# Kernel tuning notes

Hardware: AMD Instinct MI355X
Metric: run time of the kernel (lower is better)

## Reference

```python
import jax, jax.numpy as jnp
import numpy as np

DIV_EPS = 1e-7   # epsilon in dense_div denominator (as in source)
POW_EPS = 1e-7   # clamp for pow base to avoid nan (0^negative); see notes
N_OPS = 7        # [zero, one(bug:also zero), add, minus, mul, div, pow]


def setup_inputs() -> dict:
    B, S = 4096, 256
    key = jax.random.key(0)
    k1, k2, k3 = jax.random.split(key, 3)
    trans_valid = (jax.random.uniform(k1, (B, S)) < 0.7).astype(jnp.float32)
    # positive dense values so pow(h1, h0) stays real
    trans_dense = jax.random.uniform(k2, (B, S), dtype=jnp.float32)
    trans_op = jax.random.normal(k3, (B, S, N_OPS), dtype=jnp.float32)
    if_finished = jnp.zeros((B,), jnp.float32)
    if_valid = jnp.ones((B,), jnp.float32)
    return {
        "trans_valid": trans_valid,
        "trans_dense": trans_dense,
        "trans_op": trans_op,
        "if_finished": if_finished,
        "if_valid": if_valid,
        "start_pos": 0,
    }


def _shift(h):
    # matmul with next_mask ([[0,1],[0,0]]): [h0, h1] -> [0, h0]
    return jnp.stack([jnp.zeros_like(h[:, 0]), h[:, 0]], axis=-1)


def _forward(trans_valid, trans_dense, trans_op, if_finished, if_valid, start_pos):
    B, S = trans_valid.shape
    dt = trans_valid.dtype
    hold_numbers = jnp.zeros((B, 2), dt)
    hold_status = jnp.zeros((B, 2), dt)
    hold_index = jnp.zeros((B, 2), jnp.int32)
    meet_op = jnp.zeros((B,), dt)

    def step(carry, xs):
        hn, hs, hi, meet, iv, tv, td = carry
        i, op_i = xs  # i scalar, op_i [B, N_OPS]
        active = (i >= start_pos).astype(dt)  # steps before start_pos are no-ops
        tv_i = jnp.take(tv, i, axis=1)  # trans_valid[:, i]
        td_i = jnp.take(td, i, axis=1)  # trans_dense[:, i]
        itv = tv_i * (1 - meet) * (1 - if_finished) * active
        oh = jax.nn.one_hot(jnp.argmax(op_i, axis=-1), N_OPS, dtype=dt)  # [B,7]
        not_op_gate = oh[:, 0]
        dag = iv * not_op_gate * itv  # dense_applied_gate [B]
        d = dag[:, None]
        hn = d * _shift(hn) + (1 - d) * hn
        hs = d * _shift(hs) + (1 - d) * hs
        gi = dag.astype(jnp.int32)  # truncation, matches .long()
        gic = gi[:, None]
        hi = gic * jnp.stack([jnp.zeros_like(hi[:, 0]), hi[:, 0]], -1) + (1 - gic) * hi
        hi = hi.at[:, 0].set(hi[:, 0] * (1 - gi) + gi * i)
        hs = hs.at[:, 0].set(hs[:, 0] * (1 - dag) + dag)
        hn = hn.at[:, 0].set(hn[:, 0] * (1 - dag) + dag * td_i)
        op_gate = (1 - not_op_gate) * itv * iv
        meet = op_gate * (1 - meet) + meet
        iv = op_gate * hs[:, 0] * hs[:, 1] + (1 - op_gate) * iv
        h0, h1 = hn[:, 0], hn[:, 1]
        zero = jnp.zeros_like(h0)
        dense_ops = jnp.stack(
            [zero, zero,  # dense_zero, dense_one (source bug: one == zero)
             h1 + h0, h1 - h0, h1 * h0,
             h1 / (h0 + DIV_EPS),
             jnp.power(jnp.maximum(h1, POW_EPS), h0)], axis=-1)  # [B,7]
        dense_calc = jnp.sum(dense_ops * oh, axis=-1)
        fg = (1 - not_op_gate) * itv * iv  # final_op_gate (uses updated iv)
        oh2 = jax.nn.one_hot(hi[:, 0], S, dtype=dt)  # number2 position
        oh1 = jax.nn.one_hot(hi[:, 1], S, dtype=dt)  # number1 position
        fgc = fg[:, None]
        tv = tv * (1 - fgc) + tv * fgc * (1 - oh1)
        td = td * (1 - fgc) + td * fgc * (1 - oh2) + dense_calc[:, None] * fgc * oh2
        tv = tv.at[:, i].multiply(1 - fg)
        hs = hs.at[:, 0].multiply(1 - fg)
        return (hn, hs, hi, meet, iv, tv, td), None

    xs = (jnp.arange(S), jnp.moveaxis(trans_op, 1, 0))  # ([S], [S,B,7])
    carry = (hold_numbers, hold_status, hold_index, meet_op, if_valid, trans_valid, trans_dense)
    (hn, hs, hi, meet, iv, tv, td), _ = jax.lax.scan(step, carry, xs)
    ifu = iv * (1 - meet) * hs[:, 0] * (1 - hs[:, 1])
    iff = (1 - if_finished) * ifu + if_finished
    return tv, td, trans_op, iff, iv


def reference(trans_valid, trans_dense, trans_op, if_finished, if_valid, start_pos):
    return _forward(trans_valid, trans_dense, trans_op, if_finished, if_valid, start_pos)
```

## Files before the change

kernel.cpp:

```cpp
#include <hip/hip_runtime.h>

#define BB 4096
#define SS 256
#define NOPS 7

typedef float f32x4 __attribute__((ext_vector_type(4)));

__global__ __launch_bounds__(256) void arth_kernel(
    const float* __restrict__ tv_in,
    const float* __restrict__ td_in,
    const float* __restrict__ op_in,
    const float* __restrict__ if_fin,
    const float* __restrict__ if_val,
    const int* __restrict__ start_pos_p,
    float* __restrict__ out_tv,
    float* __restrict__ out_td,
    float* __restrict__ out_op,
    float* __restrict__ out_iff,
    float* __restrict__ out_iv)
{
    __shared__ float s_op[SS * NOPS];
    __shared__ float s_td[SS];
    __shared__ unsigned char s_amax[SS];
    __shared__ unsigned long long sm_op[4];
    __shared__ unsigned long long sm_num[4];

    const int b = blockIdx.x;
    const int t = threadIdx.x;
    const size_t rbase = (size_t)b * SS;
    const size_t obase = (size_t)b * (SS * NOPS);

    const int start_pos = *start_pos_p;
    const float fin_f = if_fin[b];
    const float iv0 = if_val[b];

    const f32x4* in4 = (const f32x4*)(op_in + obase);
    f32x4* o4 = (f32x4*)(out_op + obase);
    f32x4* s4 = (f32x4*)s_op;

    f32x4 v0 = in4[t];
    f32x4 v1;
    if (t < 192) v1 = in4[256 + t];
    const float tvv = tv_in[rbase + t];
    const float tdv = td_in[rbase + t];

    o4[t] = v0;
    s4[t] = v0;
    if (t < 192) {
        o4[256 + t] = v1;
        s4[256 + t] = v1;
    }
    s_td[t] = tdv;
    __syncthreads();

    int am = 0;
    float best = s_op[t * NOPS];
    #pragma unroll
    for (int k = 1; k < NOPS; ++k) {
        float v = s_op[t * NOPS + k];
        if (v > best) { best = v; am = k; }
    }
    s_amax[t] = (unsigned char)am;

    const bool validtok = (t >= start_pos) && (tvv > 0.5f);
    const bool is_num = validtok && (am == 0);
    const bool is_op = validtok && (am != 0);

    unsigned long long mo = __ballot(is_op);
    unsigned long long mn = __ballot(is_num);
    if ((t & 63) == 0) {
        sm_op[t >> 6] = mo;
        sm_num[t >> 6] = mn;
    }
    __syncthreads();

    unsigned long long w_op0 = sm_op[0], w_op1 = sm_op[1], w_op2 = sm_op[2], w_op3 = sm_op[3];
    unsigned long long w_nm[4] = { sm_num[0], sm_num[1], sm_num[2], sm_num[3] };

    int j = -1;
    if (w_op0)      j = __builtin_ctzll(w_op0);
    else if (w_op1) j = 64 + __builtin_ctzll(w_op1);
    else if (w_op2) j = 128 + __builtin_ctzll(w_op2);
    else if (w_op3) j = 192 + __builtin_ctzll(w_op3);

    int i0 = -1, i1 = -1;
    #pragma unroll
    for (int ww = 3; ww >= 0; --ww) {
        if (i1 >= 0) continue;
        unsigned long long m = w_nm[ww];
        if (j >= 0) {
            int jw = j - ww * 64;
            if (jw <= 0) m = 0ull;
            else if (jw < 64) m &= ((1ull << jw) - 1ull);
        }
        while (m && i1 < 0) {
            int bit = 63 - __builtin_clzll(m);
            if (i0 < 0) i0 = ww * 64 + bit;
            else        i1 = ww * 64 + bit;
            m &= ~(1ull << bit);
        }
    }

    const bool finished = fin_f > 0.5f;
    const bool valid0 = iv0 > 0.5f;

    float otv = tvv, otd = tdv;
    float iff, ivout;
    if (finished) {
        iff = 1.0f;
        ivout = iv0;
    } else if (!valid0) {
        iff = 0.0f;
        ivout = 0.0f;
    } else if (j < 0) {
        ivout = 1.0f;
        iff = (i0 >= 0 && i1 < 0) ? 1.0f : 0.0f;
    } else if (i1 >= 0) {
        float h0 = s_td[i0];
        float h1 = s_td[i1];
        int op = s_amax[j];
        float res;
        switch (op) {
            case 2: res = h1 + h0; break;
            case 3: res = h1 - h0; break;
            case 4: res = h1 * h0; break;
            case 5: res = h1 / (h0 + 1e-7f); break;
            case 6: res = powf(fmaxf(h1, 1e-7f), h0); break;
            default: res = 0.0f; break;
        }
        if (t == i0) otd = res;
        if (t == i1 || t == j) otv = 0.0f;
        ivout = 1.0f;
        iff = 0.0f;
    } else {
        ivout = 0.0f;
        iff = 0.0f;
    }

    out_tv[rbase + t] = otv;
    out_td[rbase + t] = otd;
    if (t == 0) {
        out_iff[b] = iff;
        out_iv[b] = ivout;
    }
}

extern "C" void kernel_launch(void* const* d_in, const int* in_sizes, int n_in,
                              void* d_out, int out_size, void* d_ws, size_t ws_size,
                              hipStream_t stream) {
    const float* tv_in = (const float*)d_in[0];
    const float* td_in = (const float*)d_in[1];
    const float* op_in = (const float*)d_in[2];
    const float* if_fin = (const float*)d_in[3];
    const float* if_val = (const float*)d_in[4];
    const int* start_pos = (const int*)d_in[5];

    float* out = (float*)d_out;
    float* out_tv = out;
    float* out_td = out + (size_t)BB * SS;
    float* out_op = out + (size_t)2 * BB * SS;
    float* out_iff = out + (size_t)9 * BB * SS;
    float* out_iv = out + (size_t)9 * BB * SS + BB;

    arth_kernel<<<BB, SS, 0, stream>>>(tv_in, td_in, op_in, if_fin, if_val,
                                       start_pos, out_tv, out_td, out_op,
                                       out_iff, out_iv);
}
```

Before: 17.46 us.

## Process one row per wavefront with register-only ballots and shuffles

```diff
diff --git a/kernel.cpp b/kernel.cpp
--- a/kernel.cpp
+++ b/kernel.cpp
@@ -6,7 +6,15 @@
 
 typedef float f32x4 __attribute__((ext_vector_type(4)));
 
-__global__ __launch_bounds__(256) void arth_kernel(
+__device__ __forceinline__ float sel4(f32x4 v, int idx) {
+    float r = v.x;
+    r = (idx == 1) ? v.y : r;
+    r = (idx == 2) ? v.z : r;
+    r = (idx == 3) ? v.w : r;
+    return r;
+}
+
+__global__ __launch_bounds__(256, 4) void arth_kernel(
     const float* __restrict__ tv_in,
     const float* __restrict__ td_in,
     const float* __restrict__ op_in,
@@ -19,108 +27,131 @@
     float* __restrict__ out_iff,
     float* __restrict__ out_iv)
 {
-    __shared__ float s_op[SS * NOPS];
-    __shared__ float s_td[SS];
-    __shared__ unsigned char s_amax[SS];
-    __shared__ unsigned long long sm_op[4];
-    __shared__ unsigned long long sm_num[4];
-
-    const int b = blockIdx.x;
     const int t = threadIdx.x;
-    const size_t rbase = (size_t)b * SS;
-    const size_t obase = (size_t)b * (SS * NOPS);
+    const int wv = t >> 6;
+    const int l  = t & 63;
+    const int r  = (blockIdx.x << 2) + wv;
+    const size_t rbase = (size_t)r * SS;
+    const size_t obase = (size_t)r * (SS * NOPS);
 
     const int start_pos = *start_pos_p;
-    const float fin_f = if_fin[b];
-    const float iv0 = if_val[b];
+    const float fin_f = if_fin[r];
+    const float iv0   = if_val[r];
 
     const f32x4* in4 = (const f32x4*)(op_in + obase);
     f32x4* o4 = (f32x4*)(out_op + obase);
-    f32x4* s4 = (f32x4*)s_op;
-
-    f32x4 v0 = in4[t];
-    f32x4 v1;
-    if (t < 192) v1 = in4[256 + t];
-    const float tvv = tv_in[rbase + t];
-    const float tdv = td_in[rbase + t];
-
-    o4[t] = v0;
-    s4[t] = v0;
-    if (t < 192) {
-        o4[256 + t] = v1;
-        s4[256 + t] = v1;
-    }
-    s_td[t] = tdv;
-    __syncthreads();
-
-    int am = 0;
-    float best = s_op[t * NOPS];
-    #pragma unroll
-    for (int k = 1; k < NOPS; ++k) {
-        float v = s_op[t * NOPS + k];
-        if (v > best) { best = v; am = k; }
-    }
-    s_amax[t] = (unsigned char)am;
-
-    const bool validtok = (t >= start_pos) && (tvv > 0.5f);
-    const bool is_num = validtok && (am == 0);
-    const bool is_op = validtok && (am != 0);
-
-    unsigned long long mo = __ballot(is_op);
-    unsigned long long mn = __ballot(is_num);
-    if ((t & 63) == 0) {
-        sm_op[t >> 6] = mo;
-        sm_num[t >> 6] = mn;
-    }
-    __syncthreads();
-
-    unsigned long long w_op0 = sm_op[0], w_op1 = sm_op[1], w_op2 = sm_op[2], w_op3 = sm_op[3];
-    unsigned long long w_nm[4] = { sm_num[0], sm_num[1], sm_num[2], sm_num[3] };
-
-    int j = -1;
-    if (w_op0)      j = __builtin_ctzll(w_op0);
-    else if (w_op1) j = 64 + __builtin_ctzll(w_op1);
-    else if (w_op2) j = 128 + __builtin_ctzll(w_op2);
-    else if (w_op3) j = 192 + __builtin_ctzll(w_op3);
-
-    int i0 = -1, i1 = -1;
-    #pragma unroll
-    for (int ww = 3; ww >= 0; --ww) {
-        if (i1 >= 0) continue;
-        unsigned long long m = w_nm[ww];
-        if (j >= 0) {
-            int jw = j - ww * 64;
-            if (jw <= 0) m = 0ull;
-            else if (jw < 64) m &= ((1ull << jw) - 1ull);
-        }
-        while (m && i1 < 0) {
-            int bit = 63 - __builtin_clzll(m);
-            if (i0 < 0) i0 = ww * 64 + bit;
-            else        i1 = ww * 64 + bit;
-            m &= ~(1ull << bit);
+
+    f32x4 c0 = in4[l];
+    f32x4 c1 = in4[l + 64];
+    f32x4 c2 = in4[l + 128];
+    f32x4 c3 = in4[l + 192];
+    f32x4 c4 = in4[l + 256];
+    f32x4 c5 = in4[l + 320];
+    f32x4 c6 = in4[l + 384];
+    const f32x4* a4 = (const f32x4*)(op_in + obase + (size_t)l * 28);
+    f32x4 u0 = a4[0], u1 = a4[1], u2 = a4[2], u3 = a4[3];
+    f32x4 u4 = a4[4], u5 = a4[5], u6 = a4[6];
+    f32x4 tv4 = *(const f32x4*)(tv_in + rbase + (l << 2));
+    f32x4 td4 = *(const f32x4*)(td_in + rbase + (l << 2));
+
+    __builtin_nontemporal_store(c0, &o4[l]);
+    __builtin_nontemporal_store(c1, &o4[l + 64]);
+    __builtin_nontemporal_store(c2, &o4[l + 128]);
+    __builtin_nontemporal_store(c3, &o4[l + 192]);
+    __builtin_nontemporal_store(c4, &o4[l + 256]);
+    __builtin_nontemporal_store(c5, &o4[l + 320]);
+    __builtin_nontemporal_store(c6, &o4[l + 384]);
+
+    float af[28];
+    *(f32x4*)(af +  0) = u0; *(f32x4*)(af +  4) = u1;
+    *(f32x4*)(af +  8) = u2; *(f32x4*)(af + 12) = u3;
+    *(f32x4*)(af + 16) = u4; *(f32x4*)(af + 20) = u5;
+    *(f32x4*)(af + 24) = u6;
+
+    int am[4];
+    #pragma unroll
+    for (int k = 0; k < 4; ++k) {
+        const int base = k * NOPS;
+        int a = 0; float best = af[base];
+        #pragma unroll
+        for (int q = 1; q < NOPS; ++q) {
+            float v = af[base + q];
+            if (v > best) { best = v; a = q; }
+        }
+        am[k] = a;
+    }
+
+    unsigned long long bop[4], bnm[4];
+    #pragma unroll
+    for (int k = 0; k < 4; ++k) {
+        const int p = (l << 2) + k;
+        const bool vt = (p >= start_pos) && (sel4(tv4, k) > 0.5f);
+        bop[k] = __ballot(vt && (am[k] != 0));
+        bnm[k] = __ballot(vt && (am[k] == 0));
+    }
+
+    int j = 1 << 30;
+    #pragma unroll
+    for (int k = 0; k < 4; ++k)
+        if (bop[k]) { int c = (__builtin_ctzll(bop[k]) << 2) + k; j = (c < j) ? c : j; }
+    const bool hasop = (j < (1 << 30));
+
+    unsigned long long msk[4];
+    #pragma unroll
+    for (int k = 0; k < 4; ++k) {
+        unsigned long long mm = bnm[k];
+        if (hasop) {
+            int lim = j - 1 - k;
+            if (lim < 0) mm = 0ull;
+            else {
+                int lmax = lim >> 2;
+                mm &= (lmax >= 63) ? ~0ull : ((2ull << lmax) - 1ull);
+            }
+        }
+        msk[k] = mm;
+    }
+
+    int i0 = -1, k0 = -1;
+    #pragma unroll
+    for (int k = 0; k < 4; ++k)
+        if (msk[k]) {
+            int c = ((63 - __builtin_clzll(msk[k])) << 2) + k;
+            if (c > i0) { i0 = c; k0 = k; }
+        }
+    int i1 = -1;
+    if (i0 >= 0) {
+        #pragma unroll
+        for (int k = 0; k < 4; ++k) {
+            unsigned long long mm = msk[k];
+            if (k == k0) mm &= ~(1ull << (i0 >> 2));
+            if (mm) {
+                int c = ((63 - __builtin_clzll(mm)) << 2) + k;
+                if (c > i1) i1 = c;
+            }
         }
     }
 
     const bool finished = fin_f > 0.5f;
     const bool valid0 = iv0 > 0.5f;
 
-    float otv = tvv, otd = tdv;
     float iff, ivout;
     if (finished) {
-        iff = 1.0f;
-        ivout = iv0;
+        iff = 1.0f; ivout = iv0;
     } else if (!valid0) {
-        iff = 0.0f;
-        ivout = 0.0f;
-    } else if (j < 0) {
-        ivout = 1.0f;
-        iff = (i0 >= 0 && i1 < 0) ? 1.0f : 0.0f;
+        iff = 0.0f; ivout = 0.0f;
+    } else if (!hasop) {
+        ivout = 1.0f; iff = (i0 >= 0 && i1 < 0) ? 1.0f : 0.0f;
     } else if (i1 >= 0) {
-        float h0 = s_td[i0];
-        float h1 = s_td[i1];
-        int op = s_amax[j];
+        float h0 = __shfl(sel4(td4, i0 & 3), i0 >> 2, 64);
+        float h1 = __shfl(sel4(td4, i1 & 3), i1 >> 2, 64);
+        int av = am[0];
+        { int ks = j & 3;
+          av = (ks == 1) ? am[1] : av;
+          av = (ks == 2) ? am[2] : av;
+          av = (ks == 3) ? am[3] : av; }
+        int opj = __shfl(av, j >> 2, 64);
         float res;
-        switch (op) {
+        switch (opj) {
             case 2: res = h1 + h0; break;
             case 3: res = h1 - h0; break;
             case 4: res = h1 * h0; break;
@@ -128,20 +159,31 @@
             case 6: res = powf(fmaxf(h1, 1e-7f), h0); break;
             default: res = 0.0f; break;
         }
-        if (t == i0) otd = res;
-        if (t == i1 || t == j) otv = 0.0f;
-        ivout = 1.0f;
-        iff = 0.0f;
+        {
+            const bool me = (l == (i0 >> 2)); const int ci = i0 & 3;
+            td4.x = (me && ci == 0) ? res : td4.x;
+            td4.y = (me && ci == 1) ? res : td4.y;
+            td4.z = (me && ci == 2) ? res : td4.z;
+            td4.w = (me && ci == 3) ? res : td4.w;
+        }
+        {
+            const bool m1 = (l == (i1 >> 2)); const int c1 = i1 & 3;
+            const bool mj = (l == (j >> 2));  const int cj = j & 3;
+            tv4.x = ((m1 && c1 == 0) || (mj && cj == 0)) ? 0.0f : tv4.x;
+            tv4.y = ((m1 && c1 == 1) || (mj && cj == 1)) ? 0.0f : tv4.y;
+            tv4.z = ((m1 && c1 == 2) || (mj && cj == 2)) ? 0.0f : tv4.z;
+            tv4.w = ((m1 && c1 == 3) || (mj && cj == 3)) ? 0.0f : tv4.w;
+        }
+        ivout = 1.0f; iff = 0.0f;
     } else {
-        ivout = 0.0f;
-        iff = 0.0f;
-    }
-
-    out_tv[rbase + t] = otv;
-    out_td[rbase + t] = otd;
-    if (t == 0) {
-        out_iff[b] = iff;
-        out_iv[b] = ivout;
+        ivout = 0.0f; iff = 0.0f;
+    }
+
+    __builtin_nontemporal_store(tv4, (f32x4*)(out_tv + rbase + (l << 2)));
+    __builtin_nontemporal_store(td4, (f32x4*)(out_td + rbase + (l << 2)));
+    if (l == 0) {
+        out_iff[r] = iff;
+        out_iv[r] = ivout;
     }
 }
 
@@ -162,7 +204,7 @@
     float* out_iff = out + (size_t)9 * BB * SS;
     float* out_iv = out + (size_t)9 * BB * SS + BB;
 
-    arth_kernel<<<BB, SS, 0, stream>>>(tv_in, td_in, op_in, if_fin, if_val,
-                                       start_pos, out_tv, out_td, out_op,
-                                       out_iff, out_iv);
+    arth_kernel<<<BB / 4, 256, 0, stream>>>(tv_in, td_in, op_in, if_fin, if_val,
+                                            start_pos, out_tv, out_td, out_op,
+                                            out_iff, out_iv);
 }
```

Measured after the change: 17.44 us. About the same (-0.1%).
